# Kernel tuning notes

Measured on AMD Instinct MI355X. Metric: run time of the kernel, lower is better.

The kernel has to match this reference:

```python
import jax, jax.numpy as jnp
import numpy as np

BERT_DIM = 768
N_ROWS = 5
N_COLS = 12
LN_EPS = 1e-5


def setup_inputs() -> dict:
    key = jax.random.key(0)
    ks = jax.random.split(key, 12)
    B, S = 256, 512
    token_hidden = jax.random.normal(ks[0], (B, S, BERT_DIM), dtype=jnp.float32)
    attention_mask = jax.random.randint(ks[1], (B, S), 0, 2, dtype=jnp.int32)
    s = lambda fan_in: 1.0 / np.sqrt(fan_in)
    return {
        "token_hidden": token_hidden,
        "attention_mask": attention_mask,
        # token_attention: Linear(768,128) -> Tanh -> Linear(128,1)
        "att_w1": jax.random.normal(ks[2], (128, BERT_DIM), dtype=jnp.float32) * s(BERT_DIM),
        "att_b1": jnp.zeros((128,), dtype=jnp.float32),
        "att_w2": jax.random.normal(ks[3], (1, 128), dtype=jnp.float32) * s(128),
        "att_b2": jnp.zeros((1,), dtype=jnp.float32),
        # feature_projector: Linear(768,256) -> GELU -> Dropout(eval) -> Linear(256,5)
        "proj_w1": jax.random.normal(ks[4], (256, BERT_DIM), dtype=jnp.float32) * s(BERT_DIM),
        "proj_b1": jnp.zeros((256,), dtype=jnp.float32),
        "proj_w2": jax.random.normal(ks[5], (N_ROWS, 256), dtype=jnp.float32) * s(256),
        "proj_b2": jnp.zeros((N_ROWS,), dtype=jnp.float32),
        # LayerNorm([5, 12])
        "ln_gamma": jnp.ones((N_ROWS, N_COLS), dtype=jnp.float32),
        "ln_beta": jnp.zeros((N_ROWS, N_COLS), dtype=jnp.float32),
    }


def reference(token_hidden, attention_mask, att_w1, att_b1, att_w2, att_b2,
              proj_w1, proj_b1, proj_w2, proj_b2, ln_gamma, ln_beta):
    # token attention scores: [B, S]
    h = jnp.tanh(jnp.einsum("bsd,hd->bsh", token_hidden, att_w1) + att_b1)
    scores = (jnp.einsum("bsh,oh->bso", h, att_w2) + att_b2)[..., 0]
    scores = jnp.where(attention_mask == 0, jnp.finfo(scores.dtype).min, scores)
    weights = jax.nn.softmax(scores, axis=-1)
    # top-k token selection (indices sorted ascending to preserve order)
    k = min(N_COLS, token_hidden.shape[1])
    _, top_idx = jax.lax.top_k(weights, k)  # [B, k]
    top_idx = jnp.sort(top_idx, axis=-1)
    selected = jnp.take_along_axis(token_hidden, top_idx[:, :, None], axis=1)  # [B, k, D]
    # feature projector (dropout is eval no-op)
    f = jax.nn.gelu(jnp.einsum("bkd,hd->bkh", selected, proj_w1) + proj_b1, approximate=False)
    f = jnp.einsum("bkh,rh->bkr", f, proj_w2) + proj_b2  # [B, k, n_rows]
    features = jnp.transpose(f, (0, 2, 1))  # [B, n_rows, k]
    if features.shape[-1] < N_COLS:
        features = jnp.pad(features, ((0, 0), (0, 0), (0, N_COLS - features.shape[-1])))
    # LayerNorm over trailing [n_rows, n_cols]
    mean = jnp.mean(features, axis=(-2, -1), keepdims=True)
    var = jnp.var(features, axis=(-2, -1), keepdims=True)
    return ln_gamma * (features - mean) * jax.lax.rsqrt(var + LN_EPS) + ln_beta
```

## Files before the change

kernel.cpp:

```cpp
#include <hip/hip_runtime.h>
#include <math.h>

#define B_BATCH 256
#define S_LEN   512
#define D_DIM   768
#define H_ATT   128
#define TOPK    12
#define NCAND   16
#define H_PROJ  256
#define N_ROWS  5
#define N_COLS  12

typedef __bf16 bf16x8 __attribute__((ext_vector_type(8)));
typedef float  f32x4  __attribute__((ext_vector_type(4)));

#define GLOBAL_AS __attribute__((address_space(1)))
#define LDS_AS    __attribute__((address_space(3)))

#define WS_SCORES 0
#define WS_WHI    524288
#define WS_WLO    720896
#define WS_W1Q    917504
#define WS_W1P    1310720

__global__ __launch_bounds__(256) void prep_kernel(
    const float* __restrict__ w1,
    const float* __restrict__ pw1,
    __bf16* __restrict__ whi, __bf16* __restrict__ wlo,
    float* __restrict__ w1q, float* __restrict__ w1p)
{
    int id = blockIdx.x * 256 + threadIdx.x;
    if (id < 98304) {
        int j    = id & 7;
        int lane = (id >> 3) & 63;
        int rest = id >> 9;
        int kt   = rest % 24;
        int nt   = rest / 24;
        int n = nt * 16 + (lane & 15);
        int k = kt * 32 + (lane >> 4) * 8 + j;
        float f = w1[n * D_DIM + k];
        __bf16 h = (__bf16)f;
        whi[id] = h;
        wlo[id] = (__bf16)(f - (float)h);
    } else if (id < 196608) {
        int e2 = id - 98304;
        int i  = e2 & 3;
        int n  = (e2 >> 2) & 127;
        int k4 = e2 >> 9;
        w1q[e2] = w1[n * D_DIM + k4 * 4 + i];
    } else {
        int e  = id - 196608;
        int i  = e & 3;
        int j  = (e >> 2) & 255;
        int k4 = e >> 10;
        w1p[e] = pw1[j * D_DIM + k4 * 4 + i];
    }
}

__device__ inline void split8(float4 a, float4 b, bf16x8& hi, bf16x8& lo) {
    float v[8] = {a.x, a.y, a.z, a.w, b.x, b.y, b.z, b.w};
#pragma unroll
    for (int i = 0; i < 8; ++i) {
        __bf16 h = (__bf16)v[i];
        hi[i] = h;
        lo[i] = (__bf16)(v[i] - (float)h);
    }
}

__global__ __launch_bounds__(256, 3) void score_mfma(
    const float*  __restrict__ th,
    const __bf16* __restrict__ whi,
    const __bf16* __restrict__ wlo,
    const float*  __restrict__ b1,
    const float*  __restrict__ w2,
    float* __restrict__ scores)
{
    __shared__ __bf16 Bs[2][2][8 * 512];

    const int tid = threadIdx.x;
    const int wv  = tid >> 6;
    const int ln  = tid & 63;

    const size_t row0 = (size_t)blockIdx.x * 128 + wv * 32 + (ln & 15);
    const float* pa0 = th + row0 * D_DIM + (ln >> 4) * 8;
    const float* pa1 = pa0 + 16 * D_DIM;

    auto stage = [&](int kt, int buf) {
#pragma unroll
        for (int q = 0; q < 4; ++q) {
            int s  = wv + q * 4;
            int hl = s >> 3;
            int nt = s & 7;
            const __bf16* src = (hl ? wlo : whi) +
                                (((size_t)nt * 24 + kt) * 64 + ln) * 8;
            __bf16* dst = &Bs[buf][hl][nt * 512];
            __builtin_amdgcn_global_load_lds(
                (GLOBAL_AS const void*)src, (LDS_AS void*)dst, 16, 0, 0);
        }
    };

    f32x4 acc[2][8];
    const f32x4 z = {0.f, 0.f, 0.f, 0.f};
#pragma unroll
    for (int i = 0; i < 2; ++i)
#pragma unroll
        for (int j = 0; j < 8; ++j) acc[i][j] = z;

    float4 c00 = *(const float4*)(pa0);
    float4 c01 = *(const float4*)(pa0 + 4);
    float4 c10 = *(const float4*)(pa1);
    float4 c11 = *(const float4*)(pa1 + 4);
    stage(0, 0);
    __syncthreads();

    for (int kt = 0; kt < 24; ++kt) {
        const int buf = kt & 1;
        float4 n00, n01, n10, n11;
        if (kt < 23) {
            n00 = *(const float4*)(pa0 + (kt + 1) * 32);
            n01 = *(const float4*)(pa0 + (kt + 1) * 32 + 4);
            n10 = *(const float4*)(pa1 + (kt + 1) * 32);
            n11 = *(const float4*)(pa1 + (kt + 1) * 32 + 4);
            stage(kt + 1, buf ^ 1);
        }

        bf16x8 ah0, al0, ah1, al1;
        split8(c00, c01, ah0, al0);
        split8(c10, c11, ah1, al1);

#pragma unroll
        for (int nt = 0; nt < 8; ++nt) {
            bf16x8 bh = *(bf16x8*)(&Bs[buf][0][nt * 512 + ln * 8]);
            bf16x8 bl = *(bf16x8*)(&Bs[buf][1][nt * 512 + ln * 8]);
            acc[0][nt] = __builtin_amdgcn_mfma_f32_16x16x32_bf16(ah0, bh, acc[0][nt], 0, 0, 0);
            acc[0][nt] = __builtin_amdgcn_mfma_f32_16x16x32_bf16(al0, bh, acc[0][nt], 0, 0, 0);
            acc[0][nt] = __builtin_amdgcn_mfma_f32_16x16x32_bf16(ah0, bl, acc[0][nt], 0, 0, 0);
            acc[1][nt] = __builtin_amdgcn_mfma_f32_16x16x32_bf16(ah1, bh, acc[1][nt], 0, 0, 0);
            acc[1][nt] = __builtin_amdgcn_mfma_f32_16x16x32_bf16(al1, bh, acc[1][nt], 0, 0, 0);
            acc[1][nt] = __builtin_amdgcn_mfma_f32_16x16x32_bf16(ah1, bl, acc[1][nt], 0, 0, 0);
        }
        if (kt < 23) {
            c00 = n00; c01 = n01; c10 = n10; c11 = n11;
            __syncthreads();
        }
    }

    const int col = ln & 15;
    float b1v[8], w2v[8];
#pragma unroll
    for (int nt = 0; nt < 8; ++nt) {
        b1v[nt] = b1[nt * 16 + col];
        w2v[nt] = w2[nt * 16 + col];
    }
    const size_t rowbase = (size_t)blockIdx.x * 128 + wv * 32;
#pragma unroll
    for (int mf = 0; mf < 2; ++mf)
#pragma unroll
        for (int r = 0; r < 4; ++r) {
            float s = 0.f;
#pragma unroll
            for (int nt = 0; nt < 8; ++nt)
                s += tanhf(acc[mf][nt][r] + b1v[nt]) * w2v[nt];
            s += __shfl_xor(s, 1, 64);
            s += __shfl_xor(s, 2, 64);
            s += __shfl_xor(s, 4, 64);
            s += __shfl_xor(s, 8, 64);
            if (col == 0)
                scores[rowbase + mf * 16 + (ln >> 4) * 4 + r] = s;
        }
}

__global__ __launch_bounds__(256) void select_kernel(
    const float* __restrict__ th,
    const int*   __restrict__ mask,
    const float* __restrict__ ascores,
    const float* __restrict__ w1q,
    const float* __restrict__ ab1,
    const float* __restrict__ aw2,
    const float* __restrict__ w1p,
    const float* __restrict__ pb1,
    const float* __restrict__ pw2,
    const float* __restrict__ pb2,
    const float* __restrict__ gamma,
    const float* __restrict__ beta,
    float* __restrict__ out)
{
    const int b   = blockIdx.x;
    const int tid = threadIdx.x;
    const int wv  = tid >> 6;
    const int ln  = tid & 63;

    __shared__ float4 xc[NCAND][192];
    __shared__ unsigned long long wtop[64];
    __shared__ int   cand[NCAND];
    __shared__ float redW[4][8];
    __shared__ float exact_sc[NCAND];
    __shared__ int   sel_slot[TOPK];
    __shared__ float gbuf[TOPK][H_PROJ + 4];
    __shared__ float feat[N_ROWS * N_COLS];
    __shared__ float stats[2];

    const float NEG_MIN = -3.402823466e38f;

    {
        int i0 = wv * 128 + ln, i1 = i0 + 64;
        float v0 = ascores[(size_t)b * S_LEN + i0];
        if (mask[(size_t)b * S_LEN + i0] == 0) v0 = NEG_MIN;
        float v1 = ascores[(size_t)b * S_LEN + i1];
        if (mask[(size_t)b * S_LEN + i1] == 0) v1 = NEG_MIN;
        unsigned k0 = __float_as_uint(v0);
        k0 = ((int)k0 >= 0) ? (k0 | 0x80000000u) : ~k0;
        unsigned k1 = __float_as_uint(v1);
        k1 = ((int)k1 >= 0) ? (k1 | 0x80000000u) : ~k1;
        unsigned long long p0 = ((unsigned long long)k0 << 32) | (0xFFFFFFFFu - (unsigned)i0);
        unsigned long long p1 = ((unsigned long long)k1 << 32) | (0xFFFFFFFFu - (unsigned)i1);
        for (int it = 0; it < NCAND; ++it) {
            unsigned long long m = p0 > p1 ? p0 : p1;
#pragma unroll
            for (int s = 1; s <= 32; s <<= 1) {
                unsigned long long o = __shfl_xor(m, s, 64);
                if (o > m) m = o;
            }
            if (ln == 0) wtop[wv * 16 + it] = m;
            if (p0 == m) p0 = 0ull;
            else if (p1 == m) p1 = 0ull;
        }
    }
    __syncthreads();
    if (wv == 0) {
        unsigned long long q = wtop[ln];
        for (int it = 0; it < NCAND; ++it) {
            unsigned long long m = q;
#pragma unroll
            for (int s = 1; s <= 32; s <<= 1) {
                unsigned long long o = __shfl_xor(m, s, 64);
                if (o > m) m = o;
            }
            if (ln == 0) cand[it] = (int)(0xFFFFFFFFu - (unsigned)(m & 0xFFFFFFFFu));
            if (q == m) q = 0ull;
        }
    }
    __syncthreads();

#pragma unroll
    for (int i = 0; i < 12; ++i) {
        int f = tid + 256 * i;
        int c = f / 192, k4 = f % 192;
        xc[c][k4] = *(const float4*)(th + ((size_t)b * S_LEN + cand[c]) * D_DIM + k4 * 4);
    }
    __syncthreads();

    {
        const int n = tid & 127;
        const int h = tid >> 7;
        float accs[8];
#pragma unroll
        for (int ci = 0; ci < 8; ++ci) accs[ci] = 0.f;
        for (int k4 = 0; k4 < 192; ++k4) {
            float4 w = *(const float4*)(w1q + (size_t)(k4 * 128 + n) * 4);
#pragma unroll
            for (int ci = 0; ci < 8; ++ci) {
                float4 x = xc[2 * ci + h][k4];
                accs[ci] += w.x * x.x + w.y * x.y + w.z * x.z + w.w * x.w;
            }
        }
        float b1n = ab1[n], w2n = aw2[n];
#pragma unroll
        for (int ci = 0; ci < 8; ++ci) {
            float val = tanhf(accs[ci] + b1n) * w2n;
            val += __shfl_xor(val, 1, 64);
            val += __shfl_xor(val, 2, 64);
            val += __shfl_xor(val, 4, 64);
            val += __shfl_xor(val, 8, 64);
            val += __shfl_xor(val, 16, 64);
            val += __shfl_xor(val, 32, 64);
            if (ln == 0) redW[wv][ci] = val;
        }
    }
    __syncthreads();
    if (tid < NCAND) {
        int c = tid;
        float ex = (c & 1) ? (redW[2][c >> 1] + redW[3][c >> 1])
                           : (redW[0][c >> 1] + redW[1][c >> 1]);
        if (mask[(size_t)b * S_LEN + cand[c]] == 0) ex = -INFINITY;
        exact_sc[c] = ex;
    }
    __syncthreads();

    if (tid == 0) {
        unsigned picked = 0;
        int slots[TOPK];
        for (int it = 0; it < TOPK; ++it) {
            float best = -INFINITY; int bslot = -1; int bidx = 1 << 30;
            for (int c = 0; c < NCAND; ++c) {
                if (picked & (1u << c)) continue;
                float e = exact_sc[c]; int idx = cand[c];
                if (e > best || (e == best && idx < bidx)) { best = e; bslot = c; bidx = idx; }
            }
            picked |= 1u << bslot;
            slots[it] = bslot;
        }
        for (int i = 1; i < TOPK; ++i) {
            int s = slots[i], key = cand[s], j = i - 1;
            while (j >= 0 && cand[slots[j]] > key) { slots[j + 1] = slots[j]; --j; }
            slots[j + 1] = s;
        }
        for (int t = 0; t < TOPK; ++t) sel_slot[t] = slots[t];
    }
    __syncthreads();

    {
        const int j = tid;
        int slots[TOPK];
#pragma unroll
        for (int t = 0; t < TOPK; ++t) slots[t] = sel_slot[t];
        float accp[TOPK];
        float bj = pb1[j];
#pragma unroll
        for (int t = 0; t < TOPK; ++t) accp[t] = bj;
        for (int k4 = 0; k4 < 192; ++k4) {
            float4 w = *(const float4*)(w1p + ((size_t)k4 * 256 + j) * 4);
#pragma unroll
            for (int t = 0; t < TOPK; ++t) {
                float4 x = xc[slots[t]][k4];
                accp[t] += w.x * x.x + w.y * x.y + w.z * x.z + w.w * x.w;
            }
        }
#pragma unroll
        for (int t = 0; t < TOPK; ++t) {
            float hh = accp[t];
            gbuf[t][j] = 0.5f * hh * (1.0f + erff(hh * 0.70710678118654752f));
        }
    }
    __syncthreads();

    if (tid < TOPK * N_ROWS) {
        int t = tid / N_ROWS, r = tid % N_ROWS;
        float s = pb2[r];
        const float4* gp = (const float4*)&gbuf[t][0];
        const float4* wp = (const float4*)(pw2 + r * H_PROJ);
        for (int q = 0; q < H_PROJ / 4; ++q) {
            float4 g = gp[q], w = wp[q];
            s += g.x * w.x + g.y * w.y + g.z * w.z + g.w * w.w;
        }
        feat[r * N_COLS + t] = s;
    }
    __syncthreads();

    if (tid == 0) {
        float sum = 0.f;
        for (int i = 0; i < N_ROWS * N_COLS; ++i) sum += feat[i];
        float mean = sum / 60.f;
        float sq = 0.f;
        for (int i = 0; i < N_ROWS * N_COLS; ++i) { float d = feat[i] - mean; sq += d * d; }
        stats[0] = mean;
        stats[1] = sq / 60.f;
    }
    __syncthreads();
    if (tid < N_ROWS * N_COLS) {
        float x = feat[tid];
        out[(size_t)b * 60 + tid] =
            gamma[tid] * (x - stats[0]) * rsqrtf(stats[1] + 1e-5f) + beta[tid];
    }
}

extern "C" void kernel_launch(void* const* d_in, const int* in_sizes, int n_in,
                              void* d_out, int out_size, void* d_ws, size_t ws_size,
                              hipStream_t stream) {
    const float* th   = (const float*)d_in[0];
    const int*   mask = (const int*)  d_in[1];
    const float* aw1  = (const float*)d_in[2];
    const float* ab1  = (const float*)d_in[3];
    const float* aw2  = (const float*)d_in[4];
    const float* pw1  = (const float*)d_in[6];
    const float* pb1  = (const float*)d_in[7];
    const float* pw2  = (const float*)d_in[8];
    const float* pb2  = (const float*)d_in[9];
    const float* gam  = (const float*)d_in[10];
    const float* bet  = (const float*)d_in[11];
    float* out = (float*)d_out;

    char* ws = (char*)d_ws;
    float*  scores = (float*)(ws + WS_SCORES);
    __bf16* whi    = (__bf16*)(ws + WS_WHI);
    __bf16* wlo    = (__bf16*)(ws + WS_WLO);
    float*  w1q    = (float*)(ws + WS_W1Q);
    float*  w1p    = (float*)(ws + WS_W1P);

    hipLaunchKernelGGL(prep_kernel, dim3(1536), dim3(256), 0, stream,
                       aw1, pw1, whi, wlo, w1q, w1p);
    hipLaunchKernelGGL(score_mfma, dim3(1024), dim3(256), 0, stream,
                       th, whi, wlo, ab1, aw2, scores);
    hipLaunchKernelGGL(select_kernel, dim3(B_BATCH), dim3(256), 0, stream,
                       th, mask, scores, w1q, ab1, aw2,
                       w1p, pb1, pw2, pb2, gam, bet, out);
}
```

Measured before the change: 726.1 us.

## Triple-buffer weight tiles and prefetch two k-steps ahead in score GEMM

Converts the score MFMA kernel from double to triple LDS buffering. Activation registers and weight tiles are now prefetched two k-steps ahead. Each iteration uses a single barrier after a partial vmcnt wait instead of a full __syncthreads at the end, so more global and LDS loads stay in flight while the MFMAs run. It costs extra LDS (48KB per block), which may limit occupancy at 3 blocks per CU, plus more live registers. Correctness depends on the hand-tuned vmcnt(8) count matching the number of outstanding loads.

```diff
diff --git a/kernel.cpp b/kernel.cpp
--- a/kernel.cpp
+++ b/kernel.cpp
@@ -75,7 +75,7 @@
     const float*  __restrict__ w2,
     float* __restrict__ scores)
 {
-    __shared__ __bf16 Bs[2][2][8 * 512];
+    __shared__ __bf16 Bs[3][2][8 * 512];
 
     const int tid = threadIdx.x;
     const int wv  = tid >> 6;
@@ -111,17 +111,25 @@
     float4 c10 = *(const float4*)(pa1);
     float4 c11 = *(const float4*)(pa1 + 4);
     stage(0, 0);
-    __syncthreads();
-
-    for (int kt = 0; kt < 24; ++kt) {
-        const int buf = kt & 1;
-        float4 n00, n01, n10, n11;
-        if (kt < 23) {
-            n00 = *(const float4*)(pa0 + (kt + 1) * 32);
-            n01 = *(const float4*)(pa0 + (kt + 1) * 32 + 4);
-            n10 = *(const float4*)(pa1 + (kt + 1) * 32);
-            n11 = *(const float4*)(pa1 + (kt + 1) * 32 + 4);
-            stage(kt + 1, buf ^ 1);
+    float4 d00 = *(const float4*)(pa0 + 32);
+    float4 d01 = *(const float4*)(pa0 + 36);
+    float4 d10 = *(const float4*)(pa1 + 32);
+    float4 d11 = *(const float4*)(pa1 + 36);
+    stage(1, 1);
+
+    int bufc = 0;
+    for (int kt = 0; kt < 23; ++kt) {
+        asm volatile("s_waitcnt vmcnt(8)" ::: "memory");
+        __builtin_amdgcn_s_barrier();
+
+        float4 e00, e01, e10, e11;
+        if (kt < 22) {
+            e00 = *(const float4*)(pa0 + (kt + 2) * 32);
+            e01 = *(const float4*)(pa0 + (kt + 2) * 32 + 4);
+            e10 = *(const float4*)(pa1 + (kt + 2) * 32);
+            e11 = *(const float4*)(pa1 + (kt + 2) * 32 + 4);
+            int buf2 = bufc + 2; if (buf2 >= 3) buf2 -= 3;
+            stage(kt + 2, buf2);
         }
 
         bf16x8 ah0, al0, ah1, al1;
@@ -130,8 +138,8 @@
 
 #pragma unroll
         for (int nt = 0; nt < 8; ++nt) {
-            bf16x8 bh = *(bf16x8*)(&Bs[buf][0][nt * 512 + ln * 8]);
-            bf16x8 bl = *(bf16x8*)(&Bs[buf][1][nt * 512 + ln * 8]);
+            bf16x8 bh = *(bf16x8*)(&Bs[bufc][0][nt * 512 + ln * 8]);
+            bf16x8 bl = *(bf16x8*)(&Bs[bufc][1][nt * 512 + ln * 8]);
             acc[0][nt] = __builtin_amdgcn_mfma_f32_16x16x32_bf16(ah0, bh, acc[0][nt], 0, 0, 0);
             acc[0][nt] = __builtin_amdgcn_mfma_f32_16x16x32_bf16(al0, bh, acc[0][nt], 0, 0, 0);
             acc[0][nt] = __builtin_amdgcn_mfma_f32_16x16x32_bf16(ah0, bl, acc[0][nt], 0, 0, 0);
@@ -139,9 +147,28 @@
             acc[1][nt] = __builtin_amdgcn_mfma_f32_16x16x32_bf16(al1, bh, acc[1][nt], 0, 0, 0);
             acc[1][nt] = __builtin_amdgcn_mfma_f32_16x16x32_bf16(ah1, bl, acc[1][nt], 0, 0, 0);
         }
-        if (kt < 23) {
-            c00 = n00; c01 = n01; c10 = n10; c11 = n11;
-            __syncthreads();
+
+        c00 = d00; c01 = d01; c10 = d10; c11 = d11;
+        if (kt < 22) { d00 = e00; d01 = e01; d10 = e10; d11 = e11; }
+        if (++bufc == 3) bufc = 0;
+    }
+
+    asm volatile("s_waitcnt vmcnt(0)" ::: "memory");
+    __builtin_amdgcn_s_barrier();
+    {
+        bf16x8 ah0, al0, ah1, al1;
+        split8(c00, c01, ah0, al0);
+        split8(c10, c11, ah1, al1);
+#pragma unroll
+        for (int nt = 0; nt < 8; ++nt) {
+            bf16x8 bh = *(bf16x8*)(&Bs[bufc][0][nt * 512 + ln * 8]);
+            bf16x8 bl = *(bf16x8*)(&Bs[bufc][1][nt * 512 + ln * 8]);
+            acc[0][nt] = __builtin_amdgcn_mfma_f32_16x16x32_bf16(ah0, bh, acc[0][nt], 0, 0, 0);
+            acc[0][nt] = __builtin_amdgcn_mfma_f32_16x16x32_bf16(al0, bh, acc[0][nt], 0, 0, 0);
+            acc[0][nt] = __builtin_amdgcn_mfma_f32_16x16x32_bf16(ah0, bl, acc[0][nt], 0, 0, 0);
+            acc[1][nt] = __builtin_amdgcn_mfma_f32_16x16x32_bf16(ah1, bh, acc[1][nt], 0, 0, 0);
+            acc[1][nt] = __builtin_amdgcn_mfma_f32_16x16x32_bf16(al1, bh, acc[1][nt], 0, 0, 0);
+            acc[1][nt] = __builtin_amdgcn_mfma_f32_16x16x32_bf16(ah1, bl, acc[1][nt], 0, 0, 0);
         }
     }
 
```

Result: no change. 733.4 us (+1.0%).
